# Performance work log

Hardware: AMD Instinct MI355X
Metric: run time of the kernel (lower is better)

Reference implementation:

```python
import jax, jax.numpy as jnp
import numpy as np

M, D, G, E = 100000, 64, 1024, 1600000  # nodes, hidden, graphs, edges


def setup_inputs() -> dict:
    key = jax.random.key(0)
    k1, k2, k3, k4 = jax.random.split(key, 4)
    x = jax.random.normal(k1, (M, D), dtype=jnp.float32)
    batch = jnp.sort(jax.random.randint(k2, (M,), 0, G)).astype(jnp.int64)
    edge = jax.random.randint(k3, (2, E), 0, M).astype(jnp.int64)
    # nn.Linear(D, 1) parameters
    att_w = jax.random.normal(k4, (1, D), dtype=jnp.float32) * (1.0 / np.sqrt(D))
    att_b = jnp.zeros((1,), dtype=jnp.float32)
    return {"x": x, "att_w": att_w, "att_b": att_b, "batch": batch, "edge": edge}


def reference(x, att_w, att_b, batch, edge):
    # imp = attention(x): [M, 1] -> [M]
    imp = (x @ att_w.T + att_b)[:, 0]
    # scatter_softmax of imp over graph segments (batch)
    seg_max = jax.ops.segment_max(imp, batch, num_segments=G)
    e = jnp.exp(imp - seg_max[batch])
    denom = jax.ops.segment_sum(e, batch, num_segments=G)
    a = e / denom[batch]  # [M]
    # (degree branch is dead code when degree=False; degree softmax unused)
    # per-node weighted outer product imp_k * x_k x_k^T, scatter-summed per graph
    wj = (a[:, None] * x)[:, :, None] * x[:, None, :]  # [M, D, D]
    out = jax.ops.segment_sum(wj, batch, num_segments=G)  # [G, D, D]
    # Triuvec: upper-triangular (incl. diagonal) vectorization, row-major
    iu = jnp.triu_indices(D)
    return out[:, iu[0], iu[1]]  # [G, D*(D+1)/2]
```

## Files before the change

### kernel.cpp

```cpp
#include <hip/hip_runtime.h>
#include <hip/hip_bf16.h>
#include <math.h>


#define DDIM 64
#define NTRI 2080
#define CAP  1024
#define TK   32

typedef __bf16 bf16x8 __attribute__((ext_vector_type(8)));
typedef float  f32x4  __attribute__((ext_vector_type(4)));

__device__ __forceinline__ float dot_row_w(const float* __restrict__ row,
                                           const float* __restrict__ sW) {
    float d = 0.f;
#pragma unroll
    for (int k = 0; k < 16; ++k) {
        const float4 v = ((const float4*)row)[k];
        const float4 w = ((const float4*)sW)[k];
        d = fmaf(v.x, w.x, d); d = fmaf(v.y, w.y, d);
        d = fmaf(v.z, w.z, d); d = fmaf(v.w, w.w, d);
    }
    return d;
}

__device__ __forceinline__ unsigned pack_bf16(float a, float b) {
    __hip_bfloat162 h2 = __float22bfloat162_rn(make_float2(a, b));
    return *reinterpret_cast<unsigned*>(&h2);
}

__global__ void __launch_bounds__(256)
bounds_kernel(const int* __restrict__ batch, int* __restrict__ seg_start, int M, int G)
{
    const int m = blockIdx.x * 256 + threadIdx.x;
    if (m >= M) return;
    const int b0 = batch[m];
    if (m == 0) {
        for (int g = 0; g <= b0; ++g) seg_start[g] = 0;
    } else {
        const int bp = batch[m - 1];
        for (int g = bp + 1; g <= b0; ++g) seg_start[g] = m;
    }
    if (m == M - 1) {
        for (int g = b0 + 1; g <= G; ++g) seg_start[g] = M;
    }
}

__global__ void __launch_bounds__(256)
sop_kernel(const float* __restrict__ x,
           const float* __restrict__ att_w,
           const float* __restrict__ att_b,
           const int*   __restrict__ seg_start,
           float*       __restrict__ out)
{
    __shared__ unsigned short sT[2][2][DDIM * TK];
    __shared__ float sA[CAP];
    __shared__ float sW[DDIM];
    __shared__ float sRed[8];

    const int g   = blockIdx.x;
    const int tid = threadIdx.x;
    const int s   = seg_start[g];
    const int n   = seg_start[g + 1] - s;
    float* og = out + (size_t)g * NTRI;

    if (n == 0) {
        for (int i = tid; i < NTRI; i += 256) og[i] = 0.f;
        return;
    }

    const int lane16 = tid & 15;
    const int grp16  = tid >> 4;
    const float4 wv  = ((const float4*)att_w)[lane16];
    const float  bb  = att_b[0];
    if (tid < DDIM) sW[tid] = att_w[tid];
    const float4* x4 = (const float4*)x;

    for (int idx = grp16; idx < n; idx += 16) {
        const float4 v = x4[(size_t)(s + idx) * 16 + lane16];
        float d = fmaf(v.x, wv.x, fmaf(v.y, wv.y, fmaf(v.z, wv.z, v.w * wv.w)));
        d += __shfl_xor(d, 1, 16);
        d += __shfl_xor(d, 2, 16);
        d += __shfl_xor(d, 4, 16);
        d += __shfl_xor(d, 8, 16);
        if (lane16 == 0 && idx < CAP) sA[idx] = d + bb;
    }
    __syncthreads();

    const int wid = tid >> 6, lane = tid & 63;
    float lmax = -INFINITY;
    for (int i = tid; i < n; i += 256) {
        const float d = (i < CAP) ? sA[i] : (dot_row_w(x + (size_t)(s + i) * DDIM, sW) + bb);
        lmax = fmaxf(lmax, d);
    }
#pragma unroll
    for (int off = 32; off > 0; off >>= 1) lmax = fmaxf(lmax, __shfl_down(lmax, off, 64));
    if (lane == 0) sRed[wid] = lmax;
    __syncthreads();
    if (tid == 0) sRed[4] = fmaxf(fmaxf(sRed[0], sRed[1]), fmaxf(sRed[2], sRed[3]));
    __syncthreads();
    const float mx = sRed[4];

    float lsum = 0.f;
    for (int i = tid; i < n; i += 256) {
        const float d  = (i < CAP) ? sA[i] : (dot_row_w(x + (size_t)(s + i) * DDIM, sW) + bb);
        const float ev = __expf(d - mx);
        if (i < CAP) sA[i] = ev;
        lsum += ev;
    }
#pragma unroll
    for (int off = 32; off > 0; off >>= 1) lsum += __shfl_down(lsum, off, 64);
    if (lane == 0) sRed[wid] = lsum;
    __syncthreads();
    if (tid == 0) sRed[5] = 1.0f / (sRed[0] + sRed[1] + sRed[2] + sRed[3]);
    __syncthreads();
    const float inv = sRed[5];
    for (int i = tid; i < CAP && i < n; i += 256) sA[i] *= inv;
    __syncthreads();

    const int pp = tid & 15;
    const int cc = tid >> 4;
    const int il = lane & 15;
    const int qd = lane >> 4;
    const int sw = qd ^ ((il >> 1) & 3);
    const int offA = (16 * wid + il) * TK + (sw << 3);
    const int offB = il * TK + (sw << 3);

    f32x4 acc[4];
#pragma unroll
    for (int jt = 0; jt < 4; ++jt) acc[jt] = (f32x4){0.f, 0.f, 0.f, 0.f};

    const int T = (n + TK - 1) / TK;
    float4 p0, p1;
    {
        const int m0 = 2 * pp;
        const float4 z = {0.f, 0.f, 0.f, 0.f};
        p0 = (m0     < n) ? x4[(size_t)(s + m0) * 16 + cc]     : z;
        p1 = (m0 + 1 < n) ? x4[(size_t)(s + m0 + 1) * 16 + cc] : z;
    }

    for (int t = 0; t < T; ++t) {
        const int t0  = t * TK;
        const int cur = t & 1;
        unsigned* A32 = (unsigned*)sT[cur][0];
        unsigned* B32 = (unsigned*)sT[cur][1];

        const int m0 = t0 + 2 * pp;
        float c0 = 0.f, c1 = 0.f;
        if (m0 < n)
            c0 = (m0 < CAP) ? sA[m0]
               : __expf(dot_row_w(x + (size_t)(s + m0) * DDIM, sW) + bb - mx) * inv;
        if (m0 + 1 < n)
            c1 = (m0 + 1 < CAP) ? sA[m0 + 1]
               : __expf(dot_row_w(x + (size_t)(s + m0 + 1) * DDIM, sW) + bb - mx) * inv;

        const float* f0 = (const float*)&p0;
        const float* f1 = (const float*)&p1;
#pragma unroll
        for (int jf = 0; jf < 4; ++jf) {
            const int f   = 4 * cc + jf;
            const int pos = (pp >> 2) ^ ((f >> 1) & 3);
            const int ui  = f * (TK / 2) + (pos << 2) + (pp & 3);
            A32[ui] = pack_bf16(c0 * f0[jf], c1 * f1[jf]);
            B32[ui] = pack_bf16(f0[jf], f1[jf]);
        }

        if (t + 1 < T) {
            const int m0n = (t + 1) * TK + 2 * pp;
            const float4 z = {0.f, 0.f, 0.f, 0.f};
            p0 = (m0n     < n) ? x4[(size_t)(s + m0n) * 16 + cc]     : z;
            p1 = (m0n + 1 < n) ? x4[(size_t)(s + m0n + 1) * 16 + cc] : z;
        }
        __syncthreads();

        const unsigned short* As = sT[cur][0];
        const unsigned short* Bs = sT[cur][1];
        const bf16x8 av = *(const bf16x8*)(As + offA);
#pragma unroll
        for (int jt = 0; jt < 4; ++jt) {
            const bf16x8 bv = *(const bf16x8*)(Bs + offB + jt * 16 * TK);
            acc[jt] = __builtin_amdgcn_mfma_f32_16x16x32_bf16(av, bv, acc[jt], 0, 0, 0);
        }
    }

    const int rbase = 16 * wid + qd * 4;
#pragma unroll
    for (int jt = 0; jt < 4; ++jt) {
        const int j = 16 * jt + il;
#pragma unroll
        for (int r = 0; r < 4; ++r) {
            const int i = rbase + r;
            if (j >= i) og[i * DDIM - (i * (i - 1)) / 2 + (j - i)] = acc[jt][r];
        }
    }
}

extern "C" void kernel_launch(void* const* d_in, const int* in_sizes, int n_in,
                              void* d_out, int out_size, void* d_ws, size_t ws_size,
                              hipStream_t stream) {
    const float* x     = (const float*)d_in[0];
    const float* att_w = (const float*)d_in[1];
    const float* att_b = (const float*)d_in[2];
    const int*   batch = (const int*)d_in[3];
    float* out = (float*)d_out;

    const int M = in_sizes[0] / DDIM;
    const int G = out_size / NTRI;

    int* seg_start = (int*)d_ws;

    bounds_kernel<<<(M + 255) / 256, 256, 0, stream>>>(batch, seg_start, M, G);
    sop_kernel<<<G, 256, 0, stream>>>(x, att_w, att_b, seg_start, out);
}
```

Before: 97.71 us.

## Drop softmax max pass and defer normalization to the output scale

Computes exp(score) directly in the first dot-product pass and accumulates the segment sum there. This removes the separate max-reduction and exp passes over shared memory, along with several block barriers. Normalization moves to a single multiply by the inverse sum when the accumulated outer products are written out. The first tile's x prefetch is also issued earlier so it overlaps the scoring pass. The cost is that softmax no longer subtracts the segment max, so large attention scores could overflow.

```diff
diff --git a/kernel.cpp b/kernel.cpp
--- a/kernel.cpp
+++ b/kernel.cpp
@@ -69,13 +69,25 @@
         return;
     }
 
+    const float4* x4 = (const float4*)x;
     const int lane16 = tid & 15;
     const int grp16  = tid >> 4;
-    const float4 wv  = ((const float4*)att_w)[lane16];
-    const float  bb  = att_b[0];
+
+    const int pp = tid & 15;
+    const int cc = tid >> 4;
+    float4 p0, p1;
+    {
+        const int m0 = 2 * pp;
+        const float4 z = {0.f, 0.f, 0.f, 0.f};
+        p0 = (m0     < n) ? x4[(size_t)(s + m0) * 16 + cc]     : z;
+        p1 = (m0 + 1 < n) ? x4[(size_t)(s + m0 + 1) * 16 + cc] : z;
+    }
+
+    const float4 wv = ((const float4*)att_w)[lane16];
+    const float  bb = att_b[0];
     if (tid < DDIM) sW[tid] = att_w[tid];
-    const float4* x4 = (const float4*)x;
 
+    float lsum = 0.f;
     for (int idx = grp16; idx < n; idx += 16) {
         const float4 v = x4[(size_t)(s + idx) * 16 + lane16];
         float d = fmaf(v.x, wv.x, fmaf(v.y, wv.y, fmaf(v.z, wv.z, v.w * wv.w)));
@@ -83,43 +95,19 @@
         d += __shfl_xor(d, 2, 16);
         d += __shfl_xor(d, 4, 16);
         d += __shfl_xor(d, 8, 16);
-        if (lane16 == 0 && idx < CAP) sA[idx] = d + bb;
+        if (lane16 == 0) {
+            const float e = __expf(d + bb);
+            if (idx < CAP) sA[idx] = e;
+            lsum += e;
+        }
     }
-    __syncthreads();
-
     const int wid = tid >> 6, lane = tid & 63;
-    float lmax = -INFINITY;
-    for (int i = tid; i < n; i += 256) {
-        const float d = (i < CAP) ? sA[i] : (dot_row_w(x + (size_t)(s + i) * DDIM, sW) + bb);
-        lmax = fmaxf(lmax, d);
-    }
-#pragma unroll
-    for (int off = 32; off > 0; off >>= 1) lmax = fmaxf(lmax, __shfl_down(lmax, off, 64));
-    if (lane == 0) sRed[wid] = lmax;
-    __syncthreads();
-    if (tid == 0) sRed[4] = fmaxf(fmaxf(sRed[0], sRed[1]), fmaxf(sRed[2], sRed[3]));
-    __syncthreads();
-    const float mx = sRed[4];
-
-    float lsum = 0.f;
-    for (int i = tid; i < n; i += 256) {
-        const float d  = (i < CAP) ? sA[i] : (dot_row_w(x + (size_t)(s + i) * DDIM, sW) + bb);
-        const float ev = __expf(d - mx);
-        if (i < CAP) sA[i] = ev;
-        lsum += ev;
-    }
 #pragma unroll
     for (int off = 32; off > 0; off >>= 1) lsum += __shfl_down(lsum, off, 64);
     if (lane == 0) sRed[wid] = lsum;
     __syncthreads();
-    if (tid == 0) sRed[5] = 1.0f / (sRed[0] + sRed[1] + sRed[2] + sRed[3]);
-    __syncthreads();
-    const float inv = sRed[5];
-    for (int i = tid; i < CAP && i < n; i += 256) sA[i] *= inv;
-    __syncthreads();
+    if (tid == 0) sRed[4] = 1.0f / (sRed[0] + sRed[1] + sRed[2] + sRed[3]);
 
-    const int pp = tid & 15;
-    const int cc = tid >> 4;
     const int il = lane & 15;
     const int qd = lane >> 4;
     const int sw = qd ^ ((il >> 1) & 3);
@@ -131,13 +119,6 @@
     for (int jt = 0; jt < 4; ++jt) acc[jt] = (f32x4){0.f, 0.f, 0.f, 0.f};
 
     const int T = (n + TK - 1) / TK;
-    float4 p0, p1;
-    {
-        const int m0 = 2 * pp;
-        const float4 z = {0.f, 0.f, 0.f, 0.f};
-        p0 = (m0     < n) ? x4[(size_t)(s + m0) * 16 + cc]     : z;
-        p1 = (m0 + 1 < n) ? x4[(size_t)(s + m0 + 1) * 16 + cc] : z;
-    }
 
     for (int t = 0; t < T; ++t) {
         const int t0  = t * TK;
@@ -149,10 +130,10 @@
         float c0 = 0.f, c1 = 0.f;
         if (m0 < n)
             c0 = (m0 < CAP) ? sA[m0]
-               : __expf(dot_row_w(x + (size_t)(s + m0) * DDIM, sW) + bb - mx) * inv;
+               : __expf(dot_row_w(x + (size_t)(s + m0) * DDIM, sW) + bb);
         if (m0 + 1 < n)
             c1 = (m0 + 1 < CAP) ? sA[m0 + 1]
-               : __expf(dot_row_w(x + (size_t)(s + m0 + 1) * DDIM, sW) + bb - mx) * inv;
+               : __expf(dot_row_w(x + (size_t)(s + m0 + 1) * DDIM, sW) + bb);
 
         const float* f0 = (const float*)&p0;
         const float* f1 = (const float*)&p1;
@@ -183,6 +164,7 @@
         }
     }
 
+    const float invd = sRed[4];
     const int rbase = 16 * wid + qd * 4;
 #pragma unroll
     for (int jt = 0; jt < 4; ++jt) {
@@ -190,7 +172,7 @@
 #pragma unroll
         for (int r = 0; r < 4; ++r) {
             const int i = rbase + r;
-            if (j >= i) og[i * DDIM - (i * (i - 1)) / 2 + (j - i)] = acc[jt][r];
+            if (j >= i) og[i * DDIM - (i * (i - 1)) / 2 + (j - i)] = acc[jt][r] * invd;
         }
     }
 }
```

New measurement: 102.3 us. +4.7%, slower.
